# Performance work log

Hardware: AMD Instinct MI355X
Metric: run time of the kernel (lower is better)

Reference implementation:

```python
import jax, jax.numpy as jnp
import numpy as np

EPS = 1e-5  # norm_eps


def setup_inputs() -> dict:
    key = jax.random.key(0)
    ks = jax.random.split(key, 9)
    N, C, T, H, W = 2, 1024, 8, 28, 28
    Di = 512
    s = 0.02  # weight init scale
    return {
        "x": jax.random.normal(ks[0], (N, C, T, H, W), jnp.float32),
        "w_theta": jax.random.normal(ks[1], (Di, C), jnp.float32) * s,
        "b_theta": jax.random.normal(ks[2], (Di,), jnp.float32) * s,
        "w_phi": jax.random.normal(ks[3], (Di, C), jnp.float32) * s,
        "b_phi": jax.random.normal(ks[4], (Di,), jnp.float32) * s,
        "w_g": jax.random.normal(ks[5], (Di, C), jnp.float32) * s,
        "b_g": jax.random.normal(ks[6], (Di,), jnp.float32) * s,
        "w_out": jax.random.normal(ks[7], (C, Di), jnp.float32) * s,
        "b_out": jax.random.normal(ks[8], (C,), jnp.float32) * s,
    }


def reference(x, w_theta, b_theta, w_phi, b_phi, w_g, b_g, w_out, b_out):
    # ProgressNL forward at step==0 (y == x), pool_size=None,
    # instantiation='softmax', norm_type='layernorm' (GroupNorm(1, C, affine=False)).
    N, C, T, H, W = x.shape
    Di = w_theta.shape[0]
    xf = x.reshape(N, C, T * H * W)  # flatten spatio-temporal tokens

    # 1x1x1 convs == per-token matmuls
    theta = jnp.einsum('dc,nct->ndt', w_theta, xf) + b_theta[None, :, None]  # [N,Di,THW]
    phi = jnp.einsum('dc,nct->ndt', w_phi, xf) + b_phi[None, :, None]
    g = jnp.einsum('dc,nct->ndt', w_g, xf) + b_g[None, :, None]

    # attention: softmax(theta^T phi / sqrt(Di)) @ g^T
    scores = jnp.einsum('nct,ncp->ntp', theta, phi) * (Di ** -0.5)  # [N,THW,THW]
    attn = jax.nn.softmax(scores, axis=-1)
    o = jnp.einsum('ntp,ncp->nct', attn, g)  # [N,Di,THW]

    # output 1x1x1 conv
    p = jnp.einsum('cd,ndt->nct', w_out, o) + b_out[None, :, None]  # [N,C,THW]

    # GroupNorm(1, C, affine=False): normalize over (C,T,H,W) per sample
    mean = jnp.mean(p, axis=(1, 2), keepdims=True)
    var = jnp.var(p, axis=(1, 2), keepdims=True)
    p = (p - mean) * jax.lax.rsqrt(var + EPS)

    return x + p.reshape(N, C, T, H, W)
```

## Files before the change

kernel.cpp:

```cpp
#include <hip/hip_runtime.h>

typedef _Float16 f16x8 __attribute__((ext_vector_type(8)));
typedef _Float16 f16x4 __attribute__((ext_vector_type(4)));
typedef float    f32x4 __attribute__((ext_vector_type(4)));

#define THW 6272
#define CCH 1024
#define DI  512

__device__ __forceinline__ void gload16(const _Float16* g, _Float16* l)
{
    __builtin_amdgcn_global_load_lds(
        (const __attribute__((address_space(1))) void*)g,
        (__attribute__((address_space(3))) void*)l, 16, 0, 0);
}

template<typename OUT_T, int BM, bool BIAS_M, bool BIAS_N, bool EXPP, bool GNP, bool RSC>
__global__ __launch_bounds__(256, 4)
void gemm_nt(const _Float16* __restrict__ A, size_t lda, size_t sAn,
             const _Float16* __restrict__ Bt, size_t ldb, size_t sBn,
             OUT_T* __restrict__ C, size_t ldc, size_t sCn,
             int K, int Kfull, float alpha,
             const float* __restrict__ bias_m,
             const float* __restrict__ bias_n,
             float* __restrict__ psum,
             const float* __restrict__ row_scale,
             int rows_ps, int stile,
             int gx, int gy)
{
    constexpr int MF = BM / 32;
    __shared__ _Float16 As[BM * 64];
    __shared__ _Float16 Bs[128 * 64];
    __shared__ float rs[4], rs2[4];
    const int tid  = threadIdx.x;
    const int lane = tid & 63;
    const int wave = tid >> 6;
    const int wr = wave >> 1, wc = wave & 1;

    const int nwg = gridDim.x;
    const int q = nwg >> 3, rr = nwg & 7;
    const int xcd = blockIdx.x & 7, seq = blockIdx.x >> 3;
    const int wg = (xcd < rr ? xcd * (q + 1) : rr * (q + 1) + (xcd - rr) * q) + seq;
    const int zz  = wg / (gx * gy);
    const int rem = wg - zz * gx * gy;
    int by, bx;
    if (stile > 0) {
        const int per = stile * stile;
        const int sgx = gx / stile;
        const int sid = rem / per, wi = rem - sid * per;
        const int srow = sid / sgx, scol = sid - srow * sgx;
        const int wrow = wi / stile;
        by = srow * stile + wrow;
        bx = scol * stile + (wi - wrow * stile);
    } else {
        by = rem / gx; bx = rem - by * gx;
    }
    const int n   = zz & 1;
    const int ks  = zz >> 1;

    const int koff = ks * K;
    const int klen = (Kfull - koff < K) ? (Kfull - koff) : K;

    A  += (size_t)n * sAn + (size_t)by * BM * lda + koff;
    Bt += (size_t)n * sBn + (size_t)bx * 128 * ldb + koff;

    const int srow = lane >> 3, sk = (lane & 7) * 8;
    const _Float16* gA = A  + (size_t)(wave * (MF * 8) + srow) * lda + sk;
    const _Float16* gB = Bt + (size_t)(wave * 32 + srow) * ldb + sk;
    _Float16* lA = As + wave * (MF * 512) + lane * 8;
    _Float16* lB = Bs + wave * 2048 + lane * 8;

    const int r  = lane & 15;
    const int kg = lane >> 4;

    f32x4 acc[MF][4] = {};

    for (int kt = 0; kt < klen; kt += 64) {
#pragma unroll
        for (int i = 0; i < MF; i++)
            gload16(gA + (size_t)(i * 8) * lda, lA + i * 512);
#pragma unroll
        for (int i = 0; i < 4; i++)
            gload16(gB + (size_t)(i * 8) * ldb, lB + i * 512);
        gA += 64; gB += 64;
        __syncthreads();
#pragma unroll
        for (int kk = 0; kk < 2; kk++) {
            f16x8 af[MF], bf[4];
#pragma unroll
            for (int mf = 0; mf < MF; mf++)
                af[mf] = *(const f16x8*)(As + (wr * (BM / 2) + mf * 16 + r) * 64 + kk * 32 + kg * 8);
#pragma unroll
            for (int nf = 0; nf < 4; nf++)
                bf[nf] = *(const f16x8*)(Bs + (wc * 64 + nf * 16 + r) * 64 + kk * 32 + kg * 8);
#pragma unroll
            for (int mf = 0; mf < MF; mf++)
#pragma unroll
                for (int nf = 0; nf < 4; nf++)
                    acc[mf][nf] = __builtin_amdgcn_mfma_f32_16x16x32_f16(
                        af[mf], bf[nf], acc[mf][nf], 0, 0, 0);
        }
        __syncthreads();
    }

    C += (size_t)zz * sCn;
    float gs = 0.f, gs2 = 0.f;

#pragma unroll
    for (int mf = 0; mf < MF; mf++) {
#pragma unroll
        for (int qi = 0; qi < 4; qi++) {
            size_t row = (size_t)by * BM + wr * (BM / 2) + mf * 16 + kg * 4 + qi;
            float bm = BIAS_M ? bias_m[row] : 0.f;
            float sc = RSC ? row_scale[(size_t)n * rows_ps + row] : 1.f;
            float rsum = 0.f;
#pragma unroll
            for (int nf = 0; nf < 4; nf++) {
                size_t col = (size_t)bx * 128 + wc * 64 + nf * 16 + r;
                float val = acc[mf][nf][qi] * alpha + bm + (BIAS_N ? bias_n[col] : 0.f);
                if (EXPP) { val = __expf(val); rsum += val; }
                else if (RSC) val *= sc;
                if (GNP) { gs += val; gs2 += val * val; }
                C[row * ldc + col] = (OUT_T)val;
            }
            if (EXPP) {
                rsum += __shfl_xor(rsum, 1);
                rsum += __shfl_xor(rsum, 2);
                rsum += __shfl_xor(rsum, 4);
                rsum += __shfl_xor(rsum, 8);
                if (r == 0)
                    psum[((size_t)n * rows_ps + row) * 98 + bx * 2 + wc] = rsum;
            }
        }
    }
    if (GNP) {
        for (int o = 32; o; o >>= 1) {
            gs  += __shfl_xor(gs, o);
            gs2 += __shfl_xor(gs2, o);
        }
        if (lane == 0) { rs[wave] = gs; rs2[wave] = gs2; }
        __syncthreads();
        if (tid == 0) {
            psum[(size_t)wg * 2]     = rs[0] + rs[1] + rs[2] + rs[3];
            psum[(size_t)wg * 2 + 1] = rs2[0] + rs2[1] + rs2[2] + rs2[3];
        }
    }
}

__global__ __launch_bounds__(256)
void rowsum_inv(const float* __restrict__ psum, float* __restrict__ inv, int nrows)
{
    int rI = blockIdx.x * 256 + threadIdx.x;
    if (rI < nrows) {
        const float* p = psum + (size_t)rI * 98;
        float s = 0.f;
#pragma unroll 7
        for (int i = 0; i < 98; i++) s += p[i];
        inv[rI] = 1.f / s;
    }
}

__global__ __launch_bounds__(256)
void combine4(const _Float16* __restrict__ Op, _Float16* __restrict__ Ot,
              int tr, int t0)
{
    const int per_n8 = tr * 64;
    int idx = blockIdx.x * 256 + threadIdx.x;
    if (idx >= 2 * per_n8) return;
    int n = idx / per_n8;
    int rem = idx - n * per_n8;
    int t = rem >> 6, d8 = rem & 63;
    const size_t slice = (size_t)tr * 512;
    float o[8] = {};
#pragma unroll
    for (int ks = 0; ks < 4; ks++) {
        f16x8 v = *(const f16x8*)(Op + (size_t)(ks * 2 + n) * slice + (size_t)rem * 8);
#pragma unroll
        for (int j = 0; j < 8; j++) o[j] += (float)v[j];
    }
    f16x8 w;
#pragma unroll
    for (int j = 0; j < 8; j++) w[j] = (_Float16)o[j];
    *(f16x8*)(Ot + ((size_t)(n * THW + t0 + t) * DI + d8 * 8)) = w;
}

__global__ __launch_bounds__(256)
void pack_weights(const float* __restrict__ wt, const float* __restrict__ wp,
                  const float* __restrict__ wg, const float* __restrict__ wo,
                  const float* __restrict__ bt, const float* __restrict__ bp,
                  _Float16* __restrict__ Wtp, _Float16* __restrict__ Wg,
                  _Float16* __restrict__ Wo, float* __restrict__ btp)
{
    int i = blockIdx.x * 256 + threadIdx.x;
    if (i < 512 * 1024) {
        Wtp[i]              = (_Float16)wt[i];
        Wtp[i + 512 * 1024] = (_Float16)wp[i];
        Wg[i]               = (_Float16)wg[i];
        Wo[i]               = (_Float16)wo[i];
    }
    if (i < 512) { btp[i] = bt[i]; btp[i + 512] = bp[i]; }
}

__global__ __launch_bounds__(256)
void transpose_cast(const float* __restrict__ x, _Float16* __restrict__ xT)
{
    __shared__ float tile[64][65];
    const int n  = blockIdx.z;
    const int t0 = blockIdx.x * 64;
    const int c0 = blockIdx.y * 64;
    const int tid = threadIdx.x;
    const float* xp = x + ((size_t)n * CCH + c0) * THW + t0;
#pragma unroll
    for (int i = 0; i < 16; i++) {
        int v = tid + i * 256;
        int c = v >> 6, t = v & 63;
        tile[t][c] = xp[(size_t)c * THW + t];
    }
    __syncthreads();
    _Float16* op = xT + ((size_t)n * THW + t0) * CCH + c0;
#pragma unroll
    for (int i = 0; i < 2; i++) {
        int v = tid + i * 256;
        int t = v >> 3, c8 = (v & 7) * 8;
        f16x8 o;
#pragma unroll
        for (int j = 0; j < 8; j++) o[j] = (_Float16)tile[t][c8 + j];
        *(f16x8*)(op + (size_t)t * CCH + c8) = o;
    }
}

__global__ __launch_bounds__(256)
void reduce_final(const float* __restrict__ partials, float* __restrict__ stats, int nblk)
{
    const int n = blockIdx.x;
    float s = 0.f, s2 = 0.f;
    for (int i = threadIdx.x; i < nblk; i += 256) {
        s  += partials[((size_t)n * nblk + i) * 2];
        s2 += partials[((size_t)n * nblk + i) * 2 + 1];
    }
    for (int o = 32; o; o >>= 1) { s += __shfl_xor(s, o); s2 += __shfl_xor(s2, o); }
    __shared__ float rs[4], rs2[4];
    if ((threadIdx.x & 63) == 0) { rs[threadIdx.x >> 6] = s; rs2[threadIdx.x >> 6] = s2; }
    __syncthreads();
    if (threadIdx.x == 0) {
        float S1 = rs[0] + rs[1] + rs[2] + rs[3];
        float S2 = rs2[0] + rs2[1] + rs2[2] + rs2[3];
        const float invc = 1.f / ((float)CCH * (float)THW);
        float mean = S1 * invc;
        float var  = S2 * invc - mean * mean;
        stats[n * 2]     = mean;
        stats[n * 2 + 1] = rsqrtf(var + 1e-5f);
    }
}

__global__ __launch_bounds__(256)
void final_residual(const float* __restrict__ x, const _Float16* __restrict__ pc16,
                    float* __restrict__ outp, const float* __restrict__ stats,
                    size_t total4)
{
    const size_t per_n4 = (size_t)CCH * THW / 4;
    for (size_t i = (size_t)blockIdx.x * 256 + threadIdx.x; i < total4;
         i += (size_t)gridDim.x * 256) {
        int n = (int)(i / per_n4);
        float mean = stats[n * 2], rstd = stats[n * 2 + 1];
        f32x4 xv = ((const f32x4*)x)[i];
        f16x4 pv = ((const f16x4*)pc16)[i];
        f32x4 ov;
#pragma unroll
        for (int j = 0; j < 4; j++) ov[j] = xv[j] + ((float)pv[j] - mean) * rstd;
        ((f32x4*)outp)[i] = ov;
    }
}

extern "C" void kernel_launch(void* const* d_in, const int* in_sizes, int n_in,
                              void* d_out, int out_size, void* d_ws, size_t ws_size,
                              hipStream_t stream)
{
    const float* x  = (const float*)d_in[0];
    const float* wt = (const float*)d_in[1];
    const float* bt = (const float*)d_in[2];
    const float* wp = (const float*)d_in[3];
    const float* bp = (const float*)d_in[4];
    const float* wg = (const float*)d_in[5];
    const float* bg = (const float*)d_in[6];
    const float* wo = (const float*)d_in[7];
    const float* bo = (const float*)d_in[8];
    float* out = (float*)d_out;

    char* ws = (char*)d_ws;
    size_t off = 0;
    auto alloc = [&](size_t b) -> void* {
        off = (off + 255) & ~(size_t)255;
        void* p = ws + off;
        off += b;
        return p;
    };

    _Float16* Wtp = (_Float16*)alloc((size_t)1024 * 1024 * 2);
    _Float16* Wg  = (_Float16*)alloc((size_t)512 * 1024 * 2);
    _Float16* Wo  = (_Float16*)alloc((size_t)1024 * 512 * 2);
    float*    btp = (float*)alloc(1024 * 4);
    _Float16* xT  = (_Float16*)alloc((size_t)2 * THW * CCH * 2);
    _Float16* tpg = (_Float16*)alloc((size_t)2 * THW * 1024 * 2);
    _Float16* g   = (_Float16*)alloc((size_t)2 * DI * THW * 2);
    _Float16* Ot  = (_Float16*)alloc((size_t)2 * THW * DI * 2);
    float*    gnp   = (float*)alloc((size_t)1568 * 2 * 4);
    float*    stats = (float*)alloc(4 * 4);

    const size_t tile_bytes = (size_t)2 * 128 * (THW * 2 + 98 * 4 + 4);
    size_t avail = (ws_size > off + 256) ? ws_size - off - 256 : 0;
    int tiles_fit = (int)(avail / tile_bytes);
    if (tiles_fit < 1) tiles_fit = 1;
    if (tiles_fit > 49) tiles_fit = 49;
    int nch = (49 + tiles_fit - 1) / tiles_fit;
    int tpc = (49 + nch - 1) / nch;

    _Float16* S    = (_Float16*)alloc((size_t)2 * tpc * 128 * THW * 2);
    float*    psum = (float*)alloc((size_t)2 * tpc * 128 * 98 * 4);
    float*    inv  = (float*)alloc((size_t)2 * tpc * 128 * 4);
    _Float16* Opart = (_Float16*)out;
    _Float16* Pc16  = tpg;

    const size_t sXT = (size_t)THW * CCH;
    const size_t sG  = (size_t)DI * THW;

    pack_weights<<<2048, 256, 0, stream>>>(wt, wp, wg, wo, bt, bp, Wtp, Wg, Wo, btp);
    transpose_cast<<<dim3(THW / 64, CCH / 64, 2), 256, 0, stream>>>(x, xT);

    gemm_nt<_Float16, 128, false, true, false, false, false><<<8 * 49 * 2, 256, 0, stream>>>(
        xT, CCH, sXT, Wtp, CCH, 0, tpg, 1024, sXT, CCH, CCH, 1.f,
        nullptr, btp, nullptr, nullptr, 0, 0, 8, 49);

    gemm_nt<_Float16, 64, true, false, false, false, false><<<49 * 8 * 2, 256, 0, stream>>>(
        Wg, CCH, 0, xT, CCH, sXT, g, THW, sG, CCH, CCH, 1.f,
        bg, nullptr, nullptr, nullptr, 0, 0, 49, 8);

    const float scale = 0.044194173824159216f;
    for (int ch = 0; ch < nch; ch++) {
        int tile0 = ch * tpc;
        int tiles = (49 - tile0 < tpc) ? (49 - tile0) : tpc;
        size_t t0 = (size_t)tile0 * 128;
        int tchRows = tiles * 128;
        int stile = (tiles % 7 == 0) ? 7 : 0;

        gemm_nt<_Float16, 128, false, false, true, false, false><<<49 * tiles * 2, 256, 0, stream>>>(
            tpg + t0 * 1024, 1024, sXT, tpg + 512, 1024, sXT,
            S, THW, (size_t)tchRows * THW, DI, DI, scale,
            nullptr, nullptr, psum, nullptr, tchRows, stile, 49, tiles);

        rowsum_inv<<<(2 * tchRows + 255) / 256, 256, 0, stream>>>(psum, inv, 2 * tchRows);

        gemm_nt<_Float16, 128, false, false, false, false, true><<<4 * tiles * 8, 256, 0, stream>>>(
            S, THW, (size_t)tchRows * THW, g, THW, sG,
            Opart, DI, (size_t)tchRows * DI, 1600, THW, 1.f,
            nullptr, nullptr, nullptr, inv, tchRows, 0, 4, tiles);

        combine4<<<(tchRows * 128 + 255) / 256, 256, 0, stream>>>(
            Opart, Ot, tchRows, (int)t0);
    }

    gemm_nt<_Float16, 128, true, false, false, true, false><<<49 * 8 * 2, 256, 0, stream>>>(
        Wo, DI, 0, Ot, DI, sG, Pc16, THW, (size_t)CCH * THW, DI, DI, 1.f,
        bo, nullptr, gnp, nullptr, 0, 0, 49, 8);

    reduce_final<<<2, 256, 0, stream>>>(gnp, stats, 392);
    final_residual<<<2048, 256, 0, stream>>>(x, Pc16, out, stats, (size_t)2 * CCH * THW / 4);
}
```

Baseline: 381.0 us.

## Double-buffer GEMM LDS tiles with K=32 stages and fold log2e into exp scale

The GEMM main loop now uses two LDS buffers of K=32 slices and issues the next slice's global-to-LDS loads before computing on the current one. It waits on partial vmcnt counts with raw barriers, so loads overlap with MFMA work instead of being serialized behind a full __syncthreads. The softmax exponent also switches to exp2f with log2(e) folded into the scale, saving a multiply per element. The risks are a halved K-step per barrier, which means more barriers, and reliance on exact vmcnt accounting. If klen/32 is odd, the loop may compute one stage too many.

```diff
diff --git a/kernel.cpp b/kernel.cpp
--- a/kernel.cpp
+++ b/kernel.cpp
@@ -28,9 +28,11 @@
              int rows_ps, int stile,
              int gx, int gy)
 {
-    constexpr int MF = BM / 32;
-    __shared__ _Float16 As[BM * 64];
-    __shared__ _Float16 Bs[128 * 64];
+    constexpr int MF   = BM / 32;
+    constexpr int AISS = BM / 64;
+    constexpr int ASZ  = BM * 32;
+    __shared__ _Float16 As[2 * ASZ];
+    __shared__ _Float16 Bs[2 * 4096];
     __shared__ float rs[4], rs2[4];
     const int tid  = threadIdx.x;
     const int lane = tid & 63;
@@ -64,43 +66,63 @@
     A  += (size_t)n * sAn + (size_t)by * BM * lda + koff;
     Bt += (size_t)n * sBn + (size_t)bx * 128 * ldb + koff;
 
-    const int srow = lane >> 3, sk = (lane & 7) * 8;
-    const _Float16* gA = A  + (size_t)(wave * (MF * 8) + srow) * lda + sk;
-    const _Float16* gB = Bt + (size_t)(wave * 32 + srow) * ldb + sk;
-    _Float16* lA = As + wave * (MF * 512) + lane * 8;
-    _Float16* lB = Bs + wave * 2048 + lane * 8;
+    const int v0 = tid, v1 = tid + 256;
+    const size_t aG0 = (size_t)(v0 >> 2) * lda + (v0 & 3) * 8;
+    const size_t aG1 = (size_t)(v1 >> 2) * lda + (v1 & 3) * 8;
+    const size_t bG0 = (size_t)(v0 >> 2) * ldb + (v0 & 3) * 8;
+    const size_t bG1 = (size_t)(v1 >> 2) * ldb + (v1 & 3) * 8;
+    const int lo0 = v0 * 8, lo1 = v1 * 8;
 
     const int r  = lane & 15;
     const int kg = lane >> 4;
 
     f32x4 acc[MF][4] = {};
 
-    for (int kt = 0; kt < klen; kt += 64) {
-#pragma unroll
-        for (int i = 0; i < MF; i++)
-            gload16(gA + (size_t)(i * 8) * lda, lA + i * 512);
-#pragma unroll
-        for (int i = 0; i < 4; i++)
-            gload16(gB + (size_t)(i * 8) * ldb, lB + i * 512);
-        gA += 64; gB += 64;
-        __syncthreads();
-#pragma unroll
-        for (int kk = 0; kk < 2; kk++) {
-            f16x8 af[MF], bf[4];
-#pragma unroll
-            for (int mf = 0; mf < MF; mf++)
-                af[mf] = *(const f16x8*)(As + (wr * (BM / 2) + mf * 16 + r) * 64 + kk * 32 + kg * 8);
+    auto STAGE = [&](int t, int b) {
+        const _Float16* a  = A  + (size_t)t * 32;
+        const _Float16* bt = Bt + (size_t)t * 32;
+        gload16(a + aG0, As + b * ASZ + lo0);
+        if constexpr (AISS == 2) gload16(a + aG1, As + b * ASZ + lo1);
+        gload16(bt + bG0, Bs + b * 4096 + lo0);
+        gload16(bt + bG1, Bs + b * 4096 + lo1);
+    };
+    auto WAITN = [&]() {
+        if constexpr (AISS == 2) asm volatile("s_waitcnt vmcnt(4)" ::: "memory");
+        else                     asm volatile("s_waitcnt vmcnt(3)" ::: "memory");
+    };
+    auto COMPUTE = [&](int b) {
+        f16x8 af[MF], bf[4];
+#pragma unroll
+        for (int mf = 0; mf < MF; mf++)
+            af[mf] = *(const f16x8*)(As + b * ASZ + (wr * (BM / 2) + mf * 16 + r) * 32 + kg * 8);
+#pragma unroll
+        for (int nf = 0; nf < 4; nf++)
+            bf[nf] = *(const f16x8*)(Bs + b * 4096 + (wc * 64 + nf * 16 + r) * 32 + kg * 8);
+#pragma unroll
+        for (int mf = 0; mf < MF; mf++)
 #pragma unroll
             for (int nf = 0; nf < 4; nf++)
-                bf[nf] = *(const f16x8*)(Bs + (wc * 64 + nf * 16 + r) * 64 + kk * 32 + kg * 8);
-#pragma unroll
-            for (int mf = 0; mf < MF; mf++)
-#pragma unroll
-                for (int nf = 0; nf < 4; nf++)
-                    acc[mf][nf] = __builtin_amdgcn_mfma_f32_16x16x32_f16(
-                        af[mf], bf[nf], acc[mf][nf], 0, 0, 0);
+                acc[mf][nf] = __builtin_amdgcn_mfma_f32_16x16x32_f16(
+                    af[mf], bf[nf], acc[mf][nf], 0, 0, 0);
+    };
+
+    const int NT = klen >> 5;
+    STAGE(0, 0);
+    for (int it = 0; it < NT; it += 2) {
+        STAGE(it + 1, 1);
+        WAITN();
+        __builtin_amdgcn_s_barrier();
+        COMPUTE(0);
+        __builtin_amdgcn_s_barrier();
+        if (it + 2 < NT) {
+            STAGE(it + 2, 0);
+            WAITN();
+        } else {
+            asm volatile("s_waitcnt vmcnt(0)" ::: "memory");
         }
-        __syncthreads();
+        __builtin_amdgcn_s_barrier();
+        COMPUTE(1);
+        __builtin_amdgcn_s_barrier();
     }
 
     C += (size_t)zz * sCn;
@@ -118,7 +140,7 @@
             for (int nf = 0; nf < 4; nf++) {
                 size_t col = (size_t)bx * 128 + wc * 64 + nf * 16 + r;
                 float val = acc[mf][nf][qi] * alpha + bm + (BIAS_N ? bias_n[col] : 0.f);
-                if (EXPP) { val = __expf(val); rsum += val; }
+                if (EXPP) { val = exp2f(val); rsum += val; }
                 else if (RSC) val *= sc;
                 if (GNP) { gs += val; gs2 += val * val; }
                 C[row * ldc + col] = (OUT_T)val;
@@ -335,7 +357,7 @@
         Wg, CCH, 0, xT, CCH, sXT, g, THW, sG, CCH, CCH, 1.f,
         bg, nullptr, nullptr, nullptr, 0, 0, 49, 8);
 
-    const float scale = 0.044194173824159216f;
+    const float scale2 = 0.044194173824159216f * 1.4426950408889634f;
     for (int ch = 0; ch < nch; ch++) {
         int tile0 = ch * tpc;
         int tiles = (49 - tile0 < tpc) ? (49 - tile0) : tpc;
@@ -345,7 +367,7 @@
 
         gemm_nt<_Float16, 128, false, false, true, false, false><<<49 * tiles * 2, 256, 0, stream>>>(
             tpg + t0 * 1024, 1024, sXT, tpg + 512, 1024, sXT,
-            S, THW, (size_t)tchRows * THW, DI, DI, scale,
+            S, THW, (size_t)tchRows * THW, DI, DI, scale2,
             nullptr, nullptr, psum, nullptr, tchRows, stile, 49, tiles);
 
         rowsum_inv<<<(2 * tchRows + 255) / 256, 256, 0, stream>>>(psum, inv, 2 * tchRows);
```

After: 381.0 us. No clear change (-0.0%).
